# Optimization experiments

Hardware: AMD Instinct MI355X
Metric: run time of the kernel (lower is better)

## Reference

```python
import jax, jax.numpy as jnp
import numpy as np

N_QUMODES = 128
N_LAYERS = 8
BATCH = 131072
HBAR = 2.0  # PennyLane default.gaussian convention; vacuum covariance = I


def setup_inputs() -> dict:
    key = jax.random.key(0)
    k1, k2 = jax.random.split(key)
    inputs = jax.random.normal(k1, (BATCH, N_QUMODES), dtype=jnp.float32)
    params = jax.random.normal(k2, (N_LAYERS, 3 * N_QUMODES), dtype=jnp.float32)
    return {"inputs": inputs, "params": params}


def _rot(theta):
    # Rotation gate on (x, p): x -> c x - s p, p -> s x + c p. Shape [..., 2, 2].
    c, s = jnp.cos(theta), jnp.sin(theta)
    return jnp.stack([jnp.stack([c, -s], -1), jnp.stack([s, c], -1)], -2)


def _build_symplectic(params):
    """Compose the full 2N x 2N symplectic matrix for all layers.

    Per layer: local per-mode blocks R(th2) @ Sq(r) @ R(th1), then a fixed
    chain of pi/4 beamsplitters on modes (0,1),(1,2),...  Quadrature ordering
    is interleaved: (x0, p0, x1, p1, ...).
    """
    N, L = N_QUMODES, N_LAYERS
    p = params.reshape(L, N, 3)
    th1, r, th2 = p[..., 0], p[..., 1], p[..., 2]
    z = jnp.zeros_like(r)
    sq = jnp.stack([jnp.stack([jnp.exp(-r), z], -1),
                    jnp.stack([z, jnp.exp(r)], -1)], -2)  # [L, N, 2, 2]
    blk = jnp.einsum('lnab,lnbc,lncd->lnad', _rot(th2), sq, _rot(th1))

    # Fixed beamsplitter chain matrix C (theta = pi/4, phi = 0).
    t = float(np.cos(np.pi / 4))
    rr = float(np.sin(np.pi / 4))
    BS4 = jnp.array([[t, 0., -rr, 0.],
                     [0., t, 0., -rr],
                     [rr, 0., t, 0.],
                     [0., rr, 0., t]], dtype=params.dtype)
    C = jnp.eye(2 * N, dtype=params.dtype)
    for i in range(N - 1):
        C = C.at[2 * i:2 * i + 4, :].set(BS4 @ C[2 * i:2 * i + 4, :])

    idx = jnp.arange(N)
    S = jnp.eye(2 * N, dtype=params.dtype)
    for l in range(L):
        D = jnp.zeros((N, 2, N, 2), params.dtype).at[idx, :, idx, :].set(blk[l])
        S = C @ (D.reshape(2 * N, 2 * N) @ S)
    return S


def reference(inputs, params):
    """Batched Gaussian simulation of the CV QNN; returns <n_i> per sample."""
    S = _build_symplectic(params)
    B, N = inputs.shape[0], N_QUMODES
    # Displacement(a, 0): mu_x += sqrt(2*hbar) * a = 2a for hbar = 2.
    mu0 = jnp.zeros((B, 2 * N), inputs.dtype).at[:, 0::2].set(2.0 * inputs)
    mu = mu0 @ S.T                      # [B, 2N]
    V = S @ S.T                         # vacuum cov = I -> V = S S^T
    dV = jnp.diagonal(V)
    dsum = dV[0::2] + dV[1::2]          # V_xx + V_pp per mode, [N]
    n = (dsum[None, :] + mu[:, 0::2] ** 2 + mu[:, 1::2] ** 2) / (2.0 * HBAR) - 0.5
    return n
```

## Files before the change

### kernel.cpp

```cpp
#include <hip/hip_runtime.h>


#define BATCH 131072
#define PSTR 40

typedef __attribute__((ext_vector_type(8))) short bf16x8;
typedef __attribute__((ext_vector_type(4))) float f32x4;

#define MFMA(a, b, c) __builtin_amdgcn_mfma_f32_16x16x32_bf16(a, b, c, 0, 0, 0)

__device__ __forceinline__ unsigned short f2bf(float f) {
  unsigned int u = __float_as_uint(f);
  u += 0x7FFFu + ((u >> 16) & 1u);
  return (unsigned short)(u >> 16);
}
__device__ __forceinline__ float bf2f(unsigned short h) {
  return __uint_as_float(((unsigned int)h) << 16);
}
__device__ __forceinline__ void pack8(const float* v, uint4& hv, uint4& lv) {
  unsigned int hw[4], lw[4];
#pragma unroll
  for (int p = 0; p < 4; ++p) {
    unsigned short h0 = f2bf(v[2 * p]), h1 = f2bf(v[2 * p + 1]);
    unsigned short l0 = f2bf(v[2 * p] - bf2f(h0)), l1 = f2bf(v[2 * p + 1] - bf2f(h1));
    hw[p] = (unsigned int)h0 | ((unsigned int)h1 << 16);
    lw[p] = (unsigned int)l0 | ((unsigned int)l1 << 16);
  }
  hv = make_uint4(hw[0], hw[1], hw[2], hw[3]);
  lv = make_uint4(lw[0], lw[1], lw[2], lw[3]);
}
__device__ __forceinline__ bf16x8 cvt8(f32x4 lo, f32x4 hi) {
  union { unsigned int u[4]; bf16x8 v; } r;
  r.u[0] = (unsigned)f2bf(lo.x) | ((unsigned)f2bf(lo.y) << 16);
  r.u[1] = (unsigned)f2bf(lo.z) | ((unsigned)f2bf(lo.w) << 16);
  r.u[2] = (unsigned)f2bf(hi.x) | ((unsigned)f2bf(hi.y) << 16);
  r.u[3] = (unsigned)f2bf(hi.z) | ((unsigned)f2bf(hi.w) << 16);
  return r.v;
}

__device__ __forceinline__ float cxf(const float* powc, int a, int nn) {
  if (a < 127) {
    if (nn == 0) return powc[a + 1];
    if (nn <= a) return powc[a - nn + 2];
    if (nn == a + 1) return -0.70710678118654752f;
    return 0.0f;
  }
  return (nn == 0) ? powc[127] : powc[128 - nn];
}

__global__ __launch_bounds__(256) void l1_prod(const float* __restrict__ params,
                                               unsigned short* __restrict__ Phi,
                                               unsigned short* __restrict__ Plo) {
  __shared__ __align__(16) char lds_raw[4 * 128 * PSTR * 2];
  __shared__ float blkA[128][4];
  __shared__ float blkB[128][4];
  __shared__ float powc[132];
  unsigned short* sLhi = (unsigned short*)lds_raw;
  unsigned short* sLlo = sLhi + 128 * PSTR;
  unsigned short* sRhi = sLlo + 128 * PSTR;
  unsigned short* sRlo = sRhi + 128 * PSTR;
  float* sEp = (float*)lds_raw;

  int bx = blockIdx.x;
  int pair = bx >> 2, tile = bx & 3;
  int tr = tile >> 1, tc = tile & 1;
  int t = threadIdx.x;
  int lane = t & 63, w = t >> 6;
  int wr = (w >> 1) * 64, wc = (w & 1) * 64;
  int l15 = lane & 15, q = lane >> 4;

  {
    int l = (t < 128) ? (2 * pair + 1) : (2 * pair);
    int nn = t & 127;
    const float* p = params + l * 384 + nn * 3;
    float th1 = p[0], r = p[1], th2 = p[2];
    float c1 = cosf(th1), s1 = sinf(th1);
    float c2 = cosf(th2), s2 = sinf(th2);
    float em = expf(-r), ep = expf(r);
    float* dst = (t < 128) ? blkA[nn] : blkB[nn];
    dst[0] = c2 * c1 * em - s2 * s1 * ep;
    dst[1] = -c2 * s1 * em - s2 * c1 * ep;
    dst[2] = s2 * c1 * em + c2 * s1 * ep;
    dst[3] = -s2 * s1 * em + c2 * c1 * ep;
    if (t < 132) powc[t] = exp2f(-0.5f * (float)t);
  }

  f32x4 acc[4][4];
#pragma unroll
  for (int a = 0; a < 4; ++a)
#pragma unroll
    for (int b = 0; b < 4; ++b) acc[a][b] = (f32x4){0.f, 0.f, 0.f, 0.f};

  for (int kc = 0; kc < 256; kc += 32) {
    __syncthreads();
#pragma unroll
    for (int it = 0; it < 2; ++it) {
      int e = it * 2048 + t * 8;
      int row = e >> 5, k0 = e & 31;
      {
        int i = tr * 128 + row;
        int a = i >> 1;
        float vv[8];
#pragma unroll
        for (int jj = 0; jj < 8; ++jj) {
          int j = kc + k0 + jj;
          int nn = j >> 1;
          vv[jj] = cxf(powc, a, nn) * blkA[nn][(i & 1) * 2 + (j & 1)];
        }
        uint4 hv, lv;
        pack8(vv, hv, lv);
        *(uint4*)(sLhi + row * PSTR + k0) = hv;
        *(uint4*)(sLlo + row * PSTR + k0) = lv;
      }
      {
        int j = tc * 128 + row;
        int nn = j >> 1;
        float b0 = blkB[nn][0 + (j & 1)];
        float b1 = blkB[nn][2 + (j & 1)];
        float vv[8];
#pragma unroll
        for (int jj = 0; jj < 8; ++jj) {
          int i = kc + k0 + jj;
          vv[jj] = cxf(powc, i >> 1, nn) * ((i & 1) ? b1 : b0);
        }
        uint4 hv, lv;
        pack8(vv, hv, lv);
        *(uint4*)(sRhi + row * PSTR + k0) = hv;
        *(uint4*)(sRlo + row * PSTR + k0) = lv;
      }
    }
    __syncthreads();
    int kb = q * 8;
    bf16x8 afh[4], afl[4], bfh[4], bfl[4];
#pragma unroll
    for (int rt = 0; rt < 4; ++rt) {
      int r = wr + rt * 16 + l15;
      afh[rt] = *(const bf16x8*)(sLhi + r * PSTR + kb);
      afl[rt] = *(const bf16x8*)(sLlo + r * PSTR + kb);
      int n = wc + rt * 16 + l15;
      bfh[rt] = *(const bf16x8*)(sRhi + n * PSTR + kb);
      bfl[rt] = *(const bf16x8*)(sRlo + n * PSTR + kb);
    }
#pragma unroll
    for (int rt = 0; rt < 4; ++rt)
#pragma unroll
      for (int ct = 0; ct < 4; ++ct) {
        acc[rt][ct] = MFMA(afh[rt], bfh[ct], acc[rt][ct]);
        acc[rt][ct] = MFMA(afh[rt], bfl[ct], acc[rt][ct]);
        acc[rt][ct] = MFMA(afl[rt], bfh[ct], acc[rt][ct]);
      }
  }

  for (int ph = 0; ph < 2; ++ph) {
    __syncthreads();
    if (wr == ph * 64) {
#pragma unroll
      for (int rt = 0; rt < 4; ++rt)
#pragma unroll
        for (int ct = 0; ct < 4; ++ct) {
          int rl = rt * 16 + q * 4;
          int col = wc + ct * 16 + l15;
#pragma unroll
          for (int rg = 0; rg < 4; ++rg) sEp[(rl + rg) * 129 + col] = acc[rt][ct][rg];
        }
    }
    __syncthreads();
    if (pair & 1) {
      int rl = t >> 2, cseg = (t & 3) * 32;
      for (int cc = 0; cc < 32; cc += 8) {
        float v[8];
#pragma unroll
        for (int jj = 0; jj < 8; ++jj) v[jj] = sEp[rl * 129 + cseg + cc + jj];
        uint4 hv, lv;
        pack8(v, hv, lv);
        int off = pair * 65536 + (tr * 128 + ph * 64 + rl) * 256 + tc * 128 + cseg + cc;
        *(uint4*)(Phi + off) = hv;
        *(uint4*)(Plo + off) = lv;
      }
    } else {
      int col = t >> 1, rseg = (t & 1) * 32;
      for (int cc = 0; cc < 32; cc += 8) {
        float v[8];
#pragma unroll
        for (int jj = 0; jj < 8; ++jj) v[jj] = sEp[(rseg + cc + jj) * 129 + col];
        uint4 hv, lv;
        pack8(v, hv, lv);
        int off = pair * 65536 + (tc * 128 + col) * 256 + tr * 128 + ph * 64 + rseg + cc;
        *(uint4*)(Phi + off) = hv;
        *(uint4*)(Plo + off) = lv;
      }
    }
  }
}

__global__ __launch_bounds__(256) void matprod(
    const unsigned short* __restrict__ Lhi_base, const unsigned short* __restrict__ Llo_base,
    unsigned short* __restrict__ Ohi, unsigned short* __restrict__ Olo) {
  __shared__ __align__(16) char lds_raw[4 * 128 * PSTR * 2];
  unsigned short* sLhi = (unsigned short*)lds_raw;
  unsigned short* sLlo = sLhi + 128 * PSTR;
  unsigned short* sRhi = sLlo + 128 * PSTR;
  unsigned short* sRlo = sRhi + 128 * PSTR;
  float* sEp = (float*)lds_raw;

  int bx = blockIdx.x;
  int pair = bx >> 2, tile = bx & 3;
  int tr = tile >> 1, tc = tile & 1;
  const unsigned short* Lhi = Lhi_base + (2 * pair + 1) * 65536;
  const unsigned short* Llo = Llo_base + (2 * pair + 1) * 65536;
  const unsigned short* Rhi = Lhi_base + (2 * pair) * 65536;
  const unsigned short* Rlo = Llo_base + (2 * pair) * 65536;

  int t = threadIdx.x;
  int lane = t & 63, w = t >> 6;
  int wr = (w >> 1) * 64, wc = (w & 1) * 64;
  int l15 = lane & 15, q = lane >> 4;

  f32x4 acc[4][4];
#pragma unroll
  for (int a = 0; a < 4; ++a)
#pragma unroll
    for (int b = 0; b < 4; ++b) acc[a][b] = (f32x4){0.f, 0.f, 0.f, 0.f};

  for (int kc = 0; kc < 256; kc += 32) {
    __syncthreads();
#pragma unroll
    for (int it = 0; it < 2; ++it) {
      int e = it * 2048 + t * 8;
      int row = e >> 5, k = e & 31;
      *(uint4*)(sLhi + row * PSTR + k) = *(const uint4*)(Lhi + (tr * 128 + row) * 256 + kc + k);
      *(uint4*)(sLlo + row * PSTR + k) = *(const uint4*)(Llo + (tr * 128 + row) * 256 + kc + k);
      *(uint4*)(sRhi + row * PSTR + k) = *(const uint4*)(Rhi + (tc * 128 + row) * 256 + kc + k);
      *(uint4*)(sRlo + row * PSTR + k) = *(const uint4*)(Rlo + (tc * 128 + row) * 256 + kc + k);
    }
    __syncthreads();
    int kb = q * 8;
    bf16x8 afh[4], afl[4], bfh[4], bfl[4];
#pragma unroll
    for (int rt = 0; rt < 4; ++rt) {
      int r = wr + rt * 16 + l15;
      afh[rt] = *(const bf16x8*)(sLhi + r * PSTR + kb);
      afl[rt] = *(const bf16x8*)(sLlo + r * PSTR + kb);
      int n = wc + rt * 16 + l15;
      bfh[rt] = *(const bf16x8*)(sRhi + n * PSTR + kb);
      bfl[rt] = *(const bf16x8*)(sRlo + n * PSTR + kb);
    }
#pragma unroll
    for (int rt = 0; rt < 4; ++rt)
#pragma unroll
      for (int ct = 0; ct < 4; ++ct) {
        acc[rt][ct] = MFMA(afh[rt], bfh[ct], acc[rt][ct]);
        acc[rt][ct] = MFMA(afh[rt], bfl[ct], acc[rt][ct]);
        acc[rt][ct] = MFMA(afl[rt], bfh[ct], acc[rt][ct]);
      }
  }

  for (int ph = 0; ph < 2; ++ph) {
    __syncthreads();
    if (wr == ph * 64) {
#pragma unroll
      for (int rt = 0; rt < 4; ++rt)
#pragma unroll
        for (int ct = 0; ct < 4; ++ct) {
          int rl = rt * 16 + q * 4;
          int col = wc + ct * 16 + l15;
#pragma unroll
          for (int rg = 0; rg < 4; ++rg) sEp[(rl + rg) * 129 + col] = acc[rt][ct][rg];
        }
    }
    __syncthreads();
    if (pair & 1) {
      int rl = t >> 2, cseg = (t & 3) * 32;
      for (int cc = 0; cc < 32; cc += 8) {
        float v[8];
#pragma unroll
        for (int jj = 0; jj < 8; ++jj) v[jj] = sEp[rl * 129 + cseg + cc + jj];
        uint4 hv, lv;
        pack8(v, hv, lv);
        int off = pair * 65536 + (tr * 128 + ph * 64 + rl) * 256 + tc * 128 + cseg + cc;
        *(uint4*)(Ohi + off) = hv;
        *(uint4*)(Olo + off) = lv;
      }
    } else {
      int col = t >> 1, rseg = (t & 1) * 32;
      for (int cc = 0; cc < 32; cc += 8) {
        float v[8];
#pragma unroll
        for (int jj = 0; jj < 8; ++jj) v[jj] = sEp[(rseg + cc + jj) * 129 + col];
        uint4 hv, lv;
        pack8(v, hv, lv);
        int off = pair * 65536 + (tc * 128 + col) * 256 + tr * 128 + ph * 64 + rseg + cc;
        *(uint4*)(Ohi + off) = hv;
        *(uint4*)(Olo + off) = lv;
      }
    }
  }
}

__global__ __launch_bounds__(256) void l3_fused(
    const unsigned short* __restrict__ Qhi, const unsigned short* __restrict__ Qlo,
    unsigned short* __restrict__ Wb, float* __restrict__ dsum_part) {
  __shared__ __align__(16) char lds_raw[4 * 128 * PSTR * 2];
  unsigned short* sLhi = (unsigned short*)lds_raw;
  unsigned short* sLlo = sLhi + 128 * PSTR;
  unsigned short* sRhi = sLlo + 128 * PSTR;
  unsigned short* sRlo = sRhi + 128 * PSTR;
  float* sEp = (float*)lds_raw;

  int tile = blockIdx.x & 3;
  int tr = tile >> 1, tc = tile & 1;
  const unsigned short* Lhi = Qhi + 65536;
  const unsigned short* Llo = Qlo + 65536;
  const unsigned short* Rhi = Qhi;
  const unsigned short* Rlo = Qlo;

  int t = threadIdx.x;
  int lane = t & 63, w = t >> 6;
  int wr = (w >> 1) * 64, wc = (w & 1) * 64;
  int l15 = lane & 15, q = lane >> 4;

  f32x4 acc[4][4];
#pragma unroll
  for (int a = 0; a < 4; ++a)
#pragma unroll
    for (int b = 0; b < 4; ++b) acc[a][b] = (f32x4){0.f, 0.f, 0.f, 0.f};

  for (int kc = 0; kc < 256; kc += 32) {
    __syncthreads();
#pragma unroll
    for (int it = 0; it < 2; ++it) {
      int e = it * 2048 + t * 8;
      int row = e >> 5, k = e & 31;
      *(uint4*)(sLhi + row * PSTR + k) = *(const uint4*)(Lhi + (tr * 128 + row) * 256 + kc + k);
      *(uint4*)(sLlo + row * PSTR + k) = *(const uint4*)(Llo + (tr * 128 + row) * 256 + kc + k);
      *(uint4*)(sRhi + row * PSTR + k) = *(const uint4*)(Rhi + (tc * 128 + row) * 256 + kc + k);
      *(uint4*)(sRlo + row * PSTR + k) = *(const uint4*)(Rlo + (tc * 128 + row) * 256 + kc + k);
    }
    __syncthreads();
    int kb = q * 8;
    bf16x8 afh[4], afl[4], bfh[4], bfl[4];
#pragma unroll
    for (int rt = 0; rt < 4; ++rt) {
      int r = wr + rt * 16 + l15;
      afh[rt] = *(const bf16x8*)(sLhi + r * PSTR + kb);
      afl[rt] = *(const bf16x8*)(sLlo + r * PSTR + kb);
      int n = wc + rt * 16 + l15;
      bfh[rt] = *(const bf16x8*)(sRhi + n * PSTR + kb);
      bfl[rt] = *(const bf16x8*)(sRlo + n * PSTR + kb);
    }
#pragma unroll
    for (int rt = 0; rt < 4; ++rt)
#pragma unroll
      for (int ct = 0; ct < 4; ++ct) {
        acc[rt][ct] = MFMA(afh[rt], bfh[ct], acc[rt][ct]);
        acc[rt][ct] = MFMA(afh[rt], bfl[ct], acc[rt][ct]);
        acc[rt][ct] = MFMA(afl[rt], bfh[ct], acc[rt][ct]);
      }
  }

  for (int ph = 0; ph < 2; ++ph) {
    __syncthreads();
    if (wr == ph * 64) {
#pragma unroll
      for (int rt = 0; rt < 4; ++rt)
#pragma unroll
        for (int ct = 0; ct < 4; ++ct) {
          int rl = rt * 16 + q * 4;
          int col = wc + ct * 16 + l15;
#pragma unroll
          for (int rg = 0; rg < 4; ++rg) sEp[(rl + rg) * 129 + col] = acc[rt][ct][rg];
        }
    }
    __syncthreads();
    int rbase = tr * 128 + ph * 64;
    int ctbase = tr * 4 + ph * 2;
#pragma unroll
    for (int ci = 0; ci < 2; ++ci) {
      int cell = w * 2 + ci;
      int c2 = cell >> 1;
      int ct = ctbase + (c2 & 1) + ((c2 & 2) ? 8 : 0);
      int ks = 2 * tc + (cell & 1);
      int n = ct * 16 + l15;
      int srow = (n < 128) ? (2 * n) : (2 * (n - 128) + 1);
      int lr = srow - rbase;
      int lc0 = (cell & 1) * 64 + q * 16;
      float v[8];
#pragma unroll
      for (int jj = 0; jj < 8; ++jj) v[jj] = 2.0f * sEp[lr * 129 + lc0 + 2 * jj];
      unsigned int wd[4];
#pragma unroll
      for (int p2 = 0; p2 < 4; ++p2)
        wd[p2] = (unsigned int)f2bf(v[2 * p2]) | ((unsigned int)f2bf(v[2 * p2 + 1]) << 16);
      *(uint4*)(Wb + ((ct * 4 + ks) * 64 + lane) * 8) = make_uint4(wd[0], wd[1], wd[2], wd[3]);
    }
    {
      int ii = t >> 3, s = t & 7;
      int c0 = s * 16;
      float sum = 0.f;
#pragma unroll
      for (int c = 0; c < 16; ++c) {
        float x = sEp[(2 * ii) * 129 + c0 + c];
        float y = sEp[(2 * ii + 1) * 129 + c0 + c];
        sum += x * x + y * y;
      }
      sum += __shfl_down(sum, 4, 8);
      sum += __shfl_down(sum, 2, 8);
      sum += __shfl_down(sum, 1, 8);
      if (s == 0) dsum_part[tc * 128 + (rbase >> 1) + ii] = sum;
    }
  }
}

__global__ __launch_bounds__(256) void qnn_gemm(
    const float* __restrict__ A, const unsigned short* __restrict__ Wb,
    const float* __restrict__ dsum_part, float* __restrict__ out) {
  int t = threadIdx.x;
  int lane = t & 63, w = t >> 6;
  int wr = w >> 1, wc = w & 1;
  int l15 = lane & 15, q = lane >> 4;
  long brow0 = (long)blockIdx.x * 64;
  long r0 = brow0 + wr * 32 + l15;

  float ds[4];
#pragma unroll
  for (int qq = 0; qq < 4; ++qq) {
    int i = (wc * 4 + qq) * 16 + l15;
    ds[qq] = dsum_part[i] + dsum_part[128 + i];
  }

  f32x4 acc[2][4][2];
#pragma unroll
  for (int rt = 0; rt < 2; ++rt)
#pragma unroll
    for (int qq = 0; qq < 4; ++qq)
#pragma unroll
      for (int xp = 0; xp < 2; ++xp) acc[rt][qq][xp] = (f32x4){0.f, 0.f, 0.f, 0.f};

  f32x4 af[4][4];
#pragma unroll
  for (int ks = 0; ks < 4; ++ks) {
    int kb = ks * 32 + q * 8;
    const float* p0 = A + r0 * 128 + kb;
    af[ks][0] = *(const f32x4*)(p0);
    af[ks][1] = *(const f32x4*)(p0 + 4);
    af[ks][2] = *(const f32x4*)(p0 + 2048);
    af[ks][3] = *(const f32x4*)(p0 + 2052);
  }

#pragma unroll
  for (int ks = 0; ks < 4; ++ks) {
    bf16x8 a0 = cvt8(af[ks][0], af[ks][1]);
    bf16x8 a1 = cvt8(af[ks][2], af[ks][3]);
#pragma unroll
    for (int qq = 0; qq < 4; ++qq)
#pragma unroll
      for (int xp = 0; xp < 2; ++xp) {
        int ct = wc * 4 + qq + 8 * xp;
        bf16x8 b = *(const bf16x8*)(Wb + ((ct * 4 + ks) * 64 + lane) * 8);
        acc[0][qq][xp] = MFMA(a0, b, acc[0][qq][xp]);
        acc[1][qq][xp] = MFMA(a1, b, acc[1][qq][xp]);
      }
  }

#pragma unroll
  for (int qq = 0; qq < 4; ++qq) {
    int i = (wc * 4 + qq) * 16 + l15;
#pragma unroll
    for (int rt = 0; rt < 2; ++rt) {
      long row0 = brow0 + wr * 32 + rt * 16 + q * 4;
      f32x4 ax = acc[rt][qq][0];
      f32x4 ap = acc[rt][qq][1];
#pragma unroll
      for (int rg = 0; rg < 4; ++rg) {
        out[(row0 + rg) * 128 + i] =
            0.25f * (ds[qq] + ax[rg] * ax[rg] + ap[rg] * ap[rg]) - 0.5f;
      }
    }
  }
}

extern "C" void kernel_launch(void* const* d_in, const int* in_sizes, int n_in,
                              void* d_out, int out_size, void* d_ws, size_t ws_size,
                              hipStream_t stream) {
  const float* inputs = (const float*)d_in[0];
  const float* params = (const float*)d_in[1];
  float* out = (float*)d_out;

  unsigned short* Phi = (unsigned short*)d_ws;
  unsigned short* Plo = Phi + 4 * 65536;
  unsigned short* Qhi = Plo + 4 * 65536;
  unsigned short* Qlo = Qhi + 2 * 65536;
  unsigned short* Wb = Qlo + 2 * 65536;
  float* dsum_part = (float*)(Wb + 65536);

  l1_prod<<<16, 256, 0, stream>>>(params, Phi, Plo);
  matprod<<<8, 256, 0, stream>>>(Phi, Plo, Qhi, Qlo);
  l3_fused<<<4, 256, 0, stream>>>(Qhi, Qlo, Wb, dsum_part);
  qnn_gemm<<<BATCH / 64, 256, 0, stream>>>(inputs, Wb, dsum_part, out);
}
```

Before: 183.9 us.

## Process multiple row chunks per block with software-prefetched input loads

Each block of the batched GEMM now handles four 64-row chunks in a loop instead of one. While the current chunk's inputs are converted to bf16 and multiplied, the next chunk's fp32 inputs are loaded into registers. The aim is to overlap global-load latency with MFMA work and to amortise per-block setup, such as the dsum reads. The cost is higher register pressure and a quarter as many blocks, which may reduce occupancy and latency hiding across the GPU.

```diff
diff --git a/kernel.cpp b/kernel.cpp
--- a/kernel.cpp
+++ b/kernel.cpp
@@ -3,6 +3,7 @@
 
 #define BATCH 131072
 #define PSTR 40
+#define NCH 4
 
 typedef __attribute__((ext_vector_type(8))) short bf16x8;
 typedef __attribute__((ext_vector_type(4))) float f32x4;
@@ -418,8 +419,8 @@
   int lane = t & 63, w = t >> 6;
   int wr = w >> 1, wc = w & 1;
   int l15 = lane & 15, q = lane >> 4;
-  long brow0 = (long)blockIdx.x * 64;
-  long r0 = brow0 + wr * 32 + l15;
+  long chunk0 = (long)blockIdx.x * NCH;
+  long r0 = chunk0 * 64 + wr * 32 + l15;
 
   float ds[4];
 #pragma unroll
@@ -428,52 +429,76 @@
     ds[qq] = dsum_part[i] + dsum_part[128 + i];
   }
 
-  f32x4 acc[2][4][2];
-#pragma unroll
-  for (int rt = 0; rt < 2; ++rt)
-#pragma unroll
-    for (int qq = 0; qq < 4; ++qq)
-#pragma unroll
-      for (int xp = 0; xp < 2; ++xp) acc[rt][qq][xp] = (f32x4){0.f, 0.f, 0.f, 0.f};
-
   f32x4 af[4][4];
-#pragma unroll
-  for (int ks = 0; ks < 4; ++ks) {
-    int kb = ks * 32 + q * 8;
-    const float* p0 = A + r0 * 128 + kb;
-    af[ks][0] = *(const f32x4*)(p0);
-    af[ks][1] = *(const f32x4*)(p0 + 4);
-    af[ks][2] = *(const f32x4*)(p0 + 2048);
-    af[ks][3] = *(const f32x4*)(p0 + 2052);
-  }
-
-#pragma unroll
-  for (int ks = 0; ks < 4; ++ks) {
-    bf16x8 a0 = cvt8(af[ks][0], af[ks][1]);
-    bf16x8 a1 = cvt8(af[ks][2], af[ks][3]);
-#pragma unroll
-    for (int qq = 0; qq < 4; ++qq)
-#pragma unroll
-      for (int xp = 0; xp < 2; ++xp) {
-        int ct = wc * 4 + qq + 8 * xp;
-        bf16x8 b = *(const bf16x8*)(Wb + ((ct * 4 + ks) * 64 + lane) * 8);
-        acc[0][qq][xp] = MFMA(a0, b, acc[0][qq][xp]);
-        acc[1][qq][xp] = MFMA(a1, b, acc[1][qq][xp]);
-      }
-  }
-
-#pragma unroll
-  for (int qq = 0; qq < 4; ++qq) {
-    int i = (wc * 4 + qq) * 16 + l15;
-#pragma unroll
-    for (int rt = 0; rt < 2; ++rt) {
-      long row0 = brow0 + wr * 32 + rt * 16 + q * 4;
-      f32x4 ax = acc[rt][qq][0];
-      f32x4 ap = acc[rt][qq][1];
-#pragma unroll
-      for (int rg = 0; rg < 4; ++rg) {
-        out[(row0 + rg) * 128 + i] =
-            0.25f * (ds[qq] + ax[rg] * ax[rg] + ap[rg] * ap[rg]) - 0.5f;
+  {
+    const float* p0 = A + r0 * 128;
+#pragma unroll
+    for (int ks = 0; ks < 4; ++ks) {
+      int kb = ks * 32 + q * 8;
+      af[ks][0] = *(const f32x4*)(p0 + kb);
+      af[ks][1] = *(const f32x4*)(p0 + kb + 4);
+      af[ks][2] = *(const f32x4*)(p0 + kb + 2048);
+      af[ks][3] = *(const f32x4*)(p0 + kb + 2052);
+    }
+  }
+
+#pragma unroll 1
+  for (int c = 0; c < NCH; ++c) {
+    long brow0 = (chunk0 + c) * 64;
+
+    bf16x8 a0f[4], a1f[4];
+#pragma unroll
+    for (int ks = 0; ks < 4; ++ks) {
+      a0f[ks] = cvt8(af[ks][0], af[ks][1]);
+      a1f[ks] = cvt8(af[ks][2], af[ks][3]);
+    }
+
+    if (c + 1 < NCH) {
+      const float* pn = A + (r0 + (long)(c + 1) * 64) * 128;
+#pragma unroll
+      for (int ks = 0; ks < 4; ++ks) {
+        int kb = ks * 32 + q * 8;
+        af[ks][0] = *(const f32x4*)(pn + kb);
+        af[ks][1] = *(const f32x4*)(pn + kb + 4);
+        af[ks][2] = *(const f32x4*)(pn + kb + 2048);
+        af[ks][3] = *(const f32x4*)(pn + kb + 2052);
+      }
+    }
+
+    f32x4 acc[2][4][2];
+#pragma unroll
+    for (int rt = 0; rt < 2; ++rt)
+#pragma unroll
+      for (int qq = 0; qq < 4; ++qq)
+#pragma unroll
+        for (int xp = 0; xp < 2; ++xp) acc[rt][qq][xp] = (f32x4){0.f, 0.f, 0.f, 0.f};
+
+#pragma unroll
+    for (int ks = 0; ks < 4; ++ks) {
+#pragma unroll
+      for (int qq = 0; qq < 4; ++qq)
+#pragma unroll
+        for (int xp = 0; xp < 2; ++xp) {
+          int ct = wc * 4 + qq + 8 * xp;
+          bf16x8 b = *(const bf16x8*)(Wb + ((ct * 4 + ks) * 64 + lane) * 8);
+          acc[0][qq][xp] = MFMA(a0f[ks], b, acc[0][qq][xp]);
+          acc[1][qq][xp] = MFMA(a1f[ks], b, acc[1][qq][xp]);
+        }
+    }
+
+#pragma unroll
+    for (int qq = 0; qq < 4; ++qq) {
+      int i = (wc * 4 + qq) * 16 + l15;
+#pragma unroll
+      for (int rt = 0; rt < 2; ++rt) {
+        long row0 = brow0 + wr * 32 + rt * 16 + q * 4;
+        f32x4 ax = acc[rt][qq][0];
+        f32x4 ap = acc[rt][qq][1];
+#pragma unroll
+        for (int rg = 0; rg < 4; ++rg) {
+          out[(row0 + rg) * 128 + i] =
+              0.25f * (ds[qq] + ax[rg] * ax[rg] + ap[rg] * ap[rg]) - 0.5f;
+        }
       }
     }
   }
@@ -496,5 +521,5 @@
   l1_prod<<<16, 256, 0, stream>>>(params, Phi, Plo);
   matprod<<<8, 256, 0, stream>>>(Phi, Plo, Qhi, Qlo);
   l3_fused<<<4, 256, 0, stream>>>(Qhi, Qlo, Wb, dsum_part);
-  qnn_gemm<<<BATCH / 64, 256, 0, stream>>>(inputs, Wb, dsum_part, out);
-}
+  qnn_gemm<<<BATCH / (64 * NCH), 256, 0, stream>>>(inputs, Wb, dsum_part, out);
+}
```

After: 180.3 us. About the same (-1.9%).
